# Performance work log

Hardware: AMD Instinct MI355X
Metric: run time of the kernel (lower is better)

The kernel has to match this reference:

```python
import jax, jax.numpy as jnp
import numpy as np

B, T, D, H = 4, 1024, 512, 8
DK = D // H
L = 2 * T - 1  # relative-position length, Transformer-XL convention


def setup_inputs() -> dict:
    key = jax.random.key(0)
    ks = jax.random.split(key, 16)
    s = 0.02  # xavier-ish init scale
    inp = {
        "query": jax.random.normal(ks[0], (B, T, D), jnp.float32),
        "key": jax.random.normal(ks[1], (B, T, D), jnp.float32),
        "value": jax.random.normal(ks[2], (B, T, D), jnp.float32),
        "pos_embedding": jax.random.normal(ks[3], (B, L, D), jnp.float32),
        "mask": jax.random.randint(ks[4], (B, T), 0, 2).astype(bool),
        # nn.Linear weights are [out, in]; y = x @ W.T + b
        "Wq": jax.random.normal(ks[5], (D, D), jnp.float32) * s,
        "bq": jnp.zeros((D,), jnp.float32),
        "Wk": jax.random.normal(ks[6], (D, D), jnp.float32) * s,
        "bk": jnp.zeros((D,), jnp.float32),
        "Wv": jax.random.normal(ks[7], (D, D), jnp.float32) * s,
        "bv": jnp.zeros((D,), jnp.float32),
        "Wr": jax.random.normal(ks[8], (D, D), jnp.float32) * s,  # rpe_proj, no bias
        "u_bias": jax.random.normal(ks[9], (H, DK), jnp.float32) * s,
        "v_bias": jax.random.normal(ks[10], (H, DK), jnp.float32) * s,
        "Wo": jax.random.normal(ks[11], (D, D), jnp.float32) * s,
        "bo": jnp.zeros((D,), jnp.float32),
    }
    return inp


def _rel_shift(x):
    # x: [B, H, T, L] -> Transformer-XL pad/reshape/slice shift, keep first L//2+1 cols
    b, h, t, l = x.shape
    x = jnp.pad(x, ((0, 0), (0, 0), (0, 0), (1, 0)))        # [B,H,T,L+1]
    x = x.reshape(b, h, l + 1, t)[:, :, 1:, :]               # drop first row
    x = x.reshape(b, h, t, l)
    return x[..., : l // 2 + 1]                              # [B,H,T,T]


def reference(query, key, value, pos_embedding, mask,
              Wq, bq, Wk, bk, Wv, bv, Wr, u_bias, v_bias, Wo, bo):
    b = query.shape[0]
    q = (query @ Wq.T + bq).reshape(b, -1, H, DK)            # [B,T,H,dk]
    k = (key @ Wk.T + bk).reshape(b, -1, H, DK)              # [B,T,H,dk]
    v = (value @ Wv.T + bv).reshape(b, -1, H, DK)            # [B,T,H,dk]
    r = (pos_embedding @ Wr.T).reshape(b, -1, H, DK)         # [B,L,H,dk]

    main = jnp.einsum('bthd,bshd->bhts', q + u_bias, k)      # content score
    rpe = jnp.einsum('bthd,blhd->bhtl', q + v_bias, r)       # [B,H,T,L]

    scores = (main + _rel_shift(rpe)) / np.sqrt(DK).astype(np.float32)
    scores = jnp.where(mask[:, None, None, :],
                       jnp.asarray(1e-4, scores.dtype), scores)
    attn = jax.nn.softmax(scores, axis=-1)                   # dropout off (eval)

    out = jnp.einsum('bhts,bshd->bhtd', attn, v)             # [B,H,T,dk]
    # Faithful to original: view(B,-1,d_model) WITHOUT transposing heads back
    out = out.reshape(b, -1, D)                              # [B,T,D] (head-interleaved)
    return out @ Wo.T + bo
```

## Files before the change

kernel.cpp:

```cpp
#include <hip/hip_runtime.h>
#include <stdint.h>
#include <stddef.h>

#define B_ 4
#define T_ 1024
#define D_ 512
#define H_ 8
#define DK_ 64
#define L_ 2047
#define LP_ 2048

typedef __attribute__((ext_vector_type(8))) short short8;
typedef __attribute__((ext_vector_type(4))) short short4_t;
typedef __attribute__((ext_vector_type(4))) float f32x4;
typedef __attribute__((ext_vector_type(4))) unsigned int u32x4;
typedef __attribute__((ext_vector_type(8))) __bf16 bf16x8;

static __device__ __forceinline__ short f2bf(float f) {
  union { float f; unsigned u; } x; x.f = f;
  unsigned r = x.u + 0x7fffu + ((x.u >> 16) & 1u);
  return (short)(r >> 16);
}

static __device__ __forceinline__ unsigned cvtpk(float lo, float hi) {
  unsigned r;
  asm("v_cvt_pk_bf16_f32 %0, %1, %2" : "=v"(r) : "v"(lo), "v"(hi));
  return r;
}

static __device__ __forceinline__ f32x4 mfma16(bf16x8 a, bf16x8 b, f32x4 c) {
  return __builtin_amdgcn_mfma_f32_16x16x32_bf16(a, b, c, 0, 0, 0);
}

static __device__ __forceinline__ bf16x8 ldbf8(const short* p) {
  return *(const bf16x8*)p;
}

__global__ __launch_bounds__(256) void convertW_kernel(
    const float* __restrict__ Wq, const float* __restrict__ Wk, const float* __restrict__ Wv,
    const float* __restrict__ Wr, const float* __restrict__ Wo,
    const unsigned char* __restrict__ mraw,
    short* __restrict__ W_bf, float* __restrict__ mask_f)
{
  if (blockIdx.x == 1280) {
    __shared__ int fmis, fany;
    if (threadIdx.x == 0) { fmis = 0; fany = 0; }
    __syncthreads();
    int lm = 0, la = 0;
    for (int i = threadIdx.x; i < B_ * T_; i += 256) {
      unsigned char c = mraw[i];
      if (c) { la = 1; if (i & 3) lm = 1; }
    }
    if (lm) atomicOr(&fmis, 1);
    if (la) atomicOr(&fany, 1);
    __syncthreads();
    int mmode = fmis ? 0 : (fany ? 1 : 2);
    const int* mi = (const int*)mraw;
    for (int i = threadIdx.x; i < B_ * T_; i += 256) {
      int mv = (mmode == 0) ? (int)mraw[i] : (mmode == 1 ? mi[i] : 0);
      mask_f[i] = mv ? 1.0f : 0.0f;
    }
    return;
  }
  int gid = blockIdx.x * 256 + threadIdx.x;
  const float* src; int base;
  if      (gid <  65536) { src = Wq; base = 0; }
  else if (gid < 131072) { src = Wk; base = 65536; }
  else if (gid < 196608) { src = Wv; base = 131072; }
  else if (gid < 262144) { src = Wr; base = 196608; }
  else                   { src = Wo; base = 262144; }
  f32x4 val = ((const f32x4*)src)[gid - base];
  short4_t o;
  o[0] = f2bf(val[0]); o[1] = f2bf(val[1]); o[2] = f2bf(val[2]); o[3] = f2bf(val[3]);
  ((short4_t*)W_bf)[gid] = o;
}

template<int VARIANT>
__global__ __launch_bounds__(256) void proj_gemm(
    const float* __restrict__ qin, const float* __restrict__ kin,
    const float* __restrict__ vin, const float* __restrict__ pin,
    const short* __restrict__ W_bf, const short* __restrict__ ao_bf,
    short* __restrict__ quO, short* __restrict__ qvO, short* __restrict__ khO,
    short* __restrict__ vtO, short* __restrict__ rhO, float* __restrict__ outF,
    const float* __restrict__ bq, const float* __restrict__ bk_,
    const float* __restrict__ bv_, const float* __restrict__ bo_,
    const float* __restrict__ ub, const float* __restrict__ vb)
{
  const int bid0 = blockIdx.x;
  constexpr int PER = (VARIANT == 0) ? 160 : 32;
  const int bid = (bid0 & 7) * PER + (bid0 >> 3);

  const float* Afp = nullptr; const short* Abf = nullptr; const short* W;
  int Mtotal, mode, m0, n0;
  if constexpr (VARIANT == 0) {
    if (bid < 768) {
      int zz = bid >> 8, r2 = bid & 255;
      m0 = (r2 >> 3) * 128; n0 = (r2 & 7) * 64;
      Afp = (zz == 0) ? qin : (zz == 1) ? kin : vin;
      W = W_bf + (size_t)zz * 262144;
      Mtotal = 4096; mode = zz;
    } else {
      int r2 = bid - 768;
      m0 = (r2 >> 3) * 128; n0 = (r2 & 7) * 64;
      Afp = pin; W = W_bf + 786432;
      Mtotal = 8188; mode = 3;
    }
  } else {
    m0 = (bid >> 3) * 128; n0 = (bid & 7) * 64;
    Abf = ao_bf; W = W_bf + 1048576;
    Mtotal = 4096; mode = 4;
  }
  __shared__ __align__(16) short As[2][128 * 64];
  __shared__ __align__(16) short Bs[2][64 * 64];
  const int tid = threadIdx.x;
  const int lane = tid & 63, wid = tid >> 6;
  const int wr = wid >> 1, wc = wid & 1;
  const int l15 = lane & 15, l4 = lane >> 4;
  const int trow = tid >> 3;
  const int s8 = tid & 7;
  const int tcolsw = ((s8 ^ (trow & 7)) << 3);
  const int wbase = wid * 512;

  f32x4 va[4][2];
  auto LOADA = [&](int kt) {
#pragma unroll
    for (int j = 0; j < 4; j++) {
      int srow = m0 + j * 32 + trow; if (srow > Mtotal - 1) srow = Mtotal - 1;
      const f32x4* p = (const f32x4*)(Afp + (size_t)srow * 512 + kt + s8 * 8);
      va[j][0] = p[0]; va[j][1] = p[1];
    }
  };
  auto WRITEA = [&](int buf) {
#pragma unroll
    for (int j = 0; j < 4; j++) {
      u32x4 wv;
      wv[0] = cvtpk(va[j][0][0], va[j][0][1]);
      wv[1] = cvtpk(va[j][0][2], va[j][0][3]);
      wv[2] = cvtpk(va[j][1][0], va[j][1][1]);
      wv[3] = cvtpk(va[j][1][2], va[j][1][3]);
      *(u32x4*)&As[buf][(j * 32 + trow) * 64 + tcolsw] = wv;
    }
  };
  auto STAGEA1 = [&](int buf, int kt) {
#pragma unroll
    for (int j = 0; j < 4; j++) {
      int srow = m0 + j * 32 + trow; if (srow > 4095) srow = 4095;
      __builtin_amdgcn_global_load_lds(
          (const __attribute__((address_space(1))) unsigned int*)(Abf + (size_t)srow * 512 + kt + tcolsw),
          (__attribute__((address_space(3))) unsigned int*)(&As[buf][j * 2048 + wbase]), 16, 0, 0);
    }
  };
  auto STAGEW = [&](int buf, int kt) {
#pragma unroll
    for (int j = 0; j < 2; j++) {
      int row = j * 32 + trow;
      __builtin_amdgcn_global_load_lds(
          (const __attribute__((address_space(1))) unsigned int*)(W + (size_t)(n0 + row) * 512 + kt + tcolsw),
          (__attribute__((address_space(3))) unsigned int*)(&Bs[buf][j * 2048 + wbase]), 16, 0, 0);
    }
  };

  f32x4 acc[4][2] = {};
  if constexpr (VARIANT == 0) { LOADA(0); STAGEW(0, 0); WRITEA(0); }
  else                        { STAGEA1(0, 0); STAGEW(0, 0); }
  __syncthreads();

  for (int it = 0; it < 8; ++it) {
    const int cur = it & 1;
    if (it < 7) {
      if constexpr (VARIANT == 0) { LOADA((it + 1) * 64); STAGEW(cur ^ 1, (it + 1) * 64); }
      else                        { STAGEA1(cur ^ 1, (it + 1) * 64); STAGEW(cur ^ 1, (it + 1) * 64); }
    }
    __builtin_amdgcn_s_setprio(1);
#pragma unroll
    for (int kf = 0; kf < 2; kf++) {
      const int colA = ((kf * 4 + l4) ^ (l15 & 7)) << 3;
      bf16x8 af[4], bf2[2];
#pragma unroll
      for (int rf = 0; rf < 4; rf++)
        af[rf] = ldbf8(&As[cur][(wr * 64 + rf * 16 + l15) * 64 + colA]);
#pragma unroll
      for (int cf = 0; cf < 2; cf++)
        bf2[cf] = ldbf8(&Bs[cur][(wc * 32 + cf * 16 + l15) * 64 + colA]);
#pragma unroll
      for (int rf = 0; rf < 4; rf++)
#pragma unroll
        for (int cf = 0; cf < 2; cf++)
          acc[rf][cf] = mfma16(af[rf], bf2[cf], acc[rf][cf]);
    }
    __builtin_amdgcn_s_setprio(0);
    if constexpr (VARIANT == 0) { if (it < 7) WRITEA(cur ^ 1); }
    __syncthreads();
  }

#pragma unroll
  for (int cf = 0; cf < 2; cf++) {
    int n = n0 + wc * 32 + cf * 16 + l15;
    float bias = 0.f, ubv = 0.f, vbv = 0.f;
    if (mode == 0) { bias = bq[n]; ubv = ub[n]; vbv = vb[n]; }
    else if (mode == 1) bias = bk_[n];
    else if (mode == 2) bias = bv_[n];
    else if (mode == 4) bias = bo_[n];
    int hh = n >> 6, dk = n & 63;
#pragma unroll
    for (int rf = 0; rf < 4; rf++) {
#pragma unroll
      for (int reg = 0; reg < 4; reg++) {
        int m = m0 + wr * 64 + rf * 16 + l4 * 4 + reg;
        float val = acc[rf][cf][reg] + bias;
        if (mode == 0) {
          int bb = m >> 10, t = m & 1023;
          size_t ad = ((size_t)(bb * H_ + hh) * T_ + t) * DK_ + dk;
          quO[ad] = f2bf(val + ubv);
          qvO[ad] = f2bf(val + vbv);
        } else if (mode == 1) {
          int bb = m >> 10, t = m & 1023;
          khO[((size_t)(bb * H_ + hh) * T_ + t) * DK_ + dk] = f2bf(val);
        } else if (mode == 2) {
          int bb = m >> 10, t = m & 1023;
          vtO[((size_t)(bb * H_ + hh) * DK_ + dk) * T_ + t] = f2bf(val);
        } else if (mode == 3) {
          if (m < B_ * L_) {
            int bb = m / L_;
            int ll = m - bb * L_;
            rhO[((size_t)(bb * H_ + hh) * LP_ + ll) * DK_ + dk] = f2bf(val);
          }
        } else {
          outF[(size_t)m * D_ + n] = val;
        }
      }
    }
  }
}

__global__ __launch_bounds__(256) void attn_kernel(
    const short* __restrict__ qu, const short* __restrict__ qv,
    const short* __restrict__ kh, const short* __restrict__ vt,
    const short* __restrict__ rh, const float* __restrict__ mask_f,
    short* __restrict__ attnout)
{
  const int tid = threadIdx.x;
  const int lane = tid & 63;
  const int w = tid >> 6;
  const int l15 = lane & 15, l4 = lane >> 4;
  const int bid = blockIdx.x;
  const int xcd = bid & 7, slot = bid >> 3;
  const int bh = (slot >> 4) * 8 + xcd;
  const int b = bh >> 3;
  const int t0b = (slot & 15) * 64;
  const int t0w = t0b + w * 16;
  const int woff = 48 - w * 16;

  __shared__ __align__(16) short Ks[2][64 * 64];
  __shared__ __align__(16) short Vs[2][64 * 64];
  __shared__ __align__(16) short Rs[2][128 * 64];
  __shared__ __align__(16) short Ps[4][16 * 64];

  const short* kB = kh + (size_t)bh * T_ * DK_;
  const short* vB = vt + (size_t)bh * DK_ * T_;
  const short* rB = rh + (size_t)bh * LP_ * DK_;
  const float* mB = mask_f + b * T_;

  const short* quB = qu + ((size_t)bh * T_ + t0w + l15) * DK_ + l4 * 8;
  const short* qvB = qv + ((size_t)bh * T_ + t0w + l15) * DK_ + l4 * 8;
  bf16x8 quf0 = ldbf8(quB), quf1 = ldbf8(quB + 32);
  bf16x8 qvf0 = ldbf8(qvB), qvf1 = ldbf8(qvB + 32);

  const short8 ones_s = {(short)0x3F80, (short)0x3F80, (short)0x3F80, (short)0x3F80,
                         (short)0x3F80, (short)0x3F80, (short)0x3F80, (short)0x3F80};
  const bf16x8 ones8 = __builtin_bit_cast(bf16x8, ones_s);

  const int trow = tid >> 3;
  const int tcol = (((tid & 7) ^ ((tid >> 3) & 7)) << 3);
  const int wbase = w * 512;

  auto STAGE = [&](int buf, int s0) {
    const int l0b = 960 + s0 - t0b;
#pragma unroll
    for (int j = 0; j < 2; j++) {
      __builtin_amdgcn_global_load_lds(
          (const __attribute__((address_space(1))) unsigned int*)(kB + (size_t)(s0 + trow + j * 32) * 64 + tcol),
          (__attribute__((address_space(3))) unsigned int*)(&Ks[buf][j * 2048 + wbase]), 16, 0, 0);
      __builtin_amdgcn_global_load_lds(
          (const __attribute__((address_space(1))) unsigned int*)(vB + (size_t)(trow + j * 32) * T_ + s0 + tcol),
          (__attribute__((address_space(3))) unsigned int*)(&Vs[buf][j * 2048 + wbase]), 16, 0, 0);
    }
#pragma unroll
    for (int j = 0; j < 4; j++) {
      __builtin_amdgcn_global_load_lds(
          (const __attribute__((address_space(1))) unsigned int*)(rB + (size_t)(l0b + trow + j * 32) * 64 + tcol),
          (__attribute__((address_space(3))) unsigned int*)(&Rs[buf][j * 2048 + wbase]), 16, 0, 0);
    }
  };

  f32x4 accO[4] = {};
  f32x4 sum_acc = {};

  STAGE(0, 0);
  __syncthreads();

  const int swz = (l15 & 7) << 3;

  for (int it = 0; it < 16; ++it) {
    const int s0 = it << 6;
    const int cur = it & 1;
    if (it < 15) STAGE(cur ^ 1, s0 + 64);

    float mk[4];
#pragma unroll
    for (int cf = 0; cf < 4; cf++) mk[cf] = mB[s0 + cf * 16 + l15];

    f32x4 sacc[4] = {};
    f32x4 gacc[5] = {};
    __builtin_amdgcn_s_setprio(1);
#pragma unroll
    for (int kf = 0; kf < 2; kf++) {
      const int col = (kf * 32 + l4 * 8) ^ swz;
      bf16x8 qf = kf ? quf1 : quf0;
      bf16x8 vf_ = kf ? qvf1 : qvf0;
#pragma unroll
      for (int cf = 0; cf < 4; cf++)
        sacc[cf] = mfma16(qf, ldbf8(&Ks[cur][(cf * 16 + l15) * 64 + col]), sacc[cf]);
#pragma unroll
      for (int gf = 0; gf < 5; gf++)
        gacc[gf] = mfma16(vf_, ldbf8(&Rs[cur][(woff + gf * 16 + l15) * 64 + col]), gacc[gf]);
    }
    __builtin_amdgcn_s_setprio(0);

    float p[4][4];
#pragma unroll
    for (int r = 0; r < 4; r++) {
      const int tl = l4 * 4 + r;
      const int e = l15 + 15 - tl;
      const int src = (lane & 48) | (e & 15);
      float sh0 = __shfl(gacc[0][r], src);
      float sh1 = __shfl(gacc[1][r], src);
      float sh2 = __shfl(gacc[2][r], src);
      float sh3 = __shfl(gacc[3][r], src);
      float sh4 = __shfl(gacc[4][r], src);
      float ga[4] = {sh0, sh1, sh2, sh3};
      float gb[4] = {sh1, sh2, sh3, sh4};
#pragma unroll
      for (int cf = 0; cf < 4; cf++) {
        float gg = (e < 16) ? ga[cf] : gb[cf];
        float lg = (sacc[cf][r] + gg) * 0.125f;
        lg = (mk[cf] != 0.f) ? 1e-4f : lg;
        p[r][cf] = __expf(lg);
      }
    }

#pragma unroll
    for (int r = 0; r < 4; r++) {
      const int tl = l4 * 4 + r;
      const int sw2 = (tl & 7) << 3;
#pragma unroll
      for (int cf = 0; cf < 4; cf++)
        Ps[w][tl * 64 + ((cf * 16 + l15) ^ sw2)] = f2bf(p[r][cf]);
    }

    __builtin_amdgcn_s_setprio(1);
#pragma unroll
    for (int kf = 0; kf < 2; kf++) {
      const int kc = kf * 32 + l4 * 8;
      bf16x8 pa = ldbf8(&Ps[w][l15 * 64 + (kc ^ swz)]);
      sum_acc = mfma16(pa, ones8, sum_acc);
#pragma unroll
      for (int vf = 0; vf < 4; vf++)
        accO[vf] = mfma16(pa, ldbf8(&Vs[cur][(vf * 16 + l15) * 64 + (kc ^ swz)]), accO[vf]);
    }
    __builtin_amdgcn_s_setprio(0);
    __syncthreads();
  }

#pragma unroll
  for (int r = 0; r < 4; r++) {
    const int tl = l4 * 4 + r;
    float inv = 1.0f / sum_acc[r];
#pragma unroll
    for (int vf = 0; vf < 4; vf++) {
      float val = accO[vf][r] * inv;
      attnout[((size_t)bh * T_ + t0w + tl) * DK_ + vf * 16 + l15] = f2bf(val);
    }
  }
}

extern "C" void kernel_launch(void* const* d_in, const int* in_sizes, int n_in,
                              void* d_out, int out_size, void* d_ws, size_t ws_size,
                              hipStream_t stream) {
  const float* qin = (const float*)d_in[0];
  const float* kin = (const float*)d_in[1];
  const float* vin = (const float*)d_in[2];
  const float* pin = (const float*)d_in[3];
  const unsigned char* mraw = (const unsigned char*)d_in[4];
  const float* Wq = (const float*)d_in[5];
  const float* bq = (const float*)d_in[6];
  const float* Wk = (const float*)d_in[7];
  const float* bk = (const float*)d_in[8];
  const float* Wv = (const float*)d_in[9];
  const float* bv = (const float*)d_in[10];
  const float* Wr = (const float*)d_in[11];
  const float* ub = (const float*)d_in[12];
  const float* vb = (const float*)d_in[13];
  const float* Wo = (const float*)d_in[14];
  const float* bo = (const float*)d_in[15];
  float* out = (float*)d_out;
  char* ws = (char*)d_ws;

  short* W_bf   = (short*)(ws + 20967424);
  float* mask_f = (float*)(ws + 23588864);
  short* quW    = (short*)(ws + 23605248);
  short* qvW    = (short*)(ws + 27799552);
  short* khW    = (short*)(ws + 31993856);
  short* vtW    = (short*)(ws + 36188160);
  short* rhW    = (short*)(ws + 40382464);
  short* aoW    = (short*)(ws + 48771072);

  convertW_kernel<<<dim3(1281), dim3(256), 0, stream>>>(
      Wq, Wk, Wv, Wr, Wo, mraw, W_bf, mask_f);
  proj_gemm<0><<<dim3(1280), dim3(256), 0, stream>>>(
      qin, kin, vin, pin, W_bf, aoW, quW, qvW, khW, vtW, rhW, nullptr,
      bq, bk, bv, bo, ub, vb);
  attn_kernel<<<dim3(512), dim3(256), 0, stream>>>(
      quW, qvW, khW, vtW, rhW, mask_f, aoW);
  proj_gemm<1><<<dim3(256), dim3(256), 0, stream>>>(
      qin, kin, vin, pin, W_bf, aoW, quW, qvW, khW, vtW, rhW, out,
      bq, bk, bv, bo, ub, vb);
}
```

Measured before the change: 97.12 us.

## Load projection weights directly into registers instead of staging through LDS

The projection GEMM no longer stages the weight tile in shared memory. Each lane now loads its MFMA B-fragments straight from global memory into registers, which drops the Bs buffer and halves LDS use. The Wo variant switches from async global_load_lds to register loads followed by LDS writes, the k-loop is fully unrolled, and launch bounds now request 4 blocks per CU for higher occupancy. In exchange, the weight loads are issued in the same iteration that consumes them, so their latency is no longer hidden by the double buffer, and register pressure rises.

```diff
diff --git a/kernel.cpp b/kernel.cpp
--- a/kernel.cpp
+++ b/kernel.cpp
@@ -76,7 +76,7 @@
 }
 
 template<int VARIANT>
-__global__ __launch_bounds__(256) void proj_gemm(
+__global__ __launch_bounds__(256, 4) void proj_gemm(
     const float* __restrict__ qin, const float* __restrict__ kin,
     const float* __restrict__ vin, const float* __restrict__ pin,
     const short* __restrict__ W_bf, const short* __restrict__ ao_bf,
@@ -111,7 +111,6 @@
     Mtotal = 4096; mode = 4;
   }
   __shared__ __align__(16) short As[2][128 * 64];
-  __shared__ __align__(16) short Bs[2][64 * 64];
   const int tid = threadIdx.x;
   const int lane = tid & 63, wid = tid >> 6;
   const int wr = wid >> 1, wc = wid & 1;
@@ -119,77 +118,78 @@
   const int trow = tid >> 3;
   const int s8 = tid & 7;
   const int tcolsw = ((s8 ^ (trow & 7)) << 3);
-  const int wbase = wid * 512;
+
+  const short* Wp0 = W + (size_t)(n0 + wc * 32 + l15) * 512 + l4 * 8;
+  const short* Wp1 = W + (size_t)(n0 + wc * 32 + 16 + l15) * 512 + l4 * 8;
 
   f32x4 va[4][2];
+  bf16x8 va1[4];
+  bf16x8 wf[2][2];
+
   auto LOADA = [&](int kt) {
-#pragma unroll
-    for (int j = 0; j < 4; j++) {
-      int srow = m0 + j * 32 + trow; if (srow > Mtotal - 1) srow = Mtotal - 1;
-      const f32x4* p = (const f32x4*)(Afp + (size_t)srow * 512 + kt + s8 * 8);
-      va[j][0] = p[0]; va[j][1] = p[1];
-    }
+    if constexpr (VARIANT == 0) {
+#pragma unroll
+      for (int j = 0; j < 4; j++) {
+        int srow = m0 + j * 32 + trow; if (srow > Mtotal - 1) srow = Mtotal - 1;
+        const f32x4* p = (const f32x4*)(Afp + (size_t)srow * 512 + kt + s8 * 8);
+        va[j][0] = p[0]; va[j][1] = p[1];
+      }
+    } else {
+#pragma unroll
+      for (int j = 0; j < 4; j++) {
+        int srow = m0 + j * 32 + trow; if (srow > 4095) srow = 4095;
+        va1[j] = ldbf8(Abf + (size_t)srow * 512 + kt + s8 * 8);
+      }
+    }
+  };
+  auto LOADW = [&](int kt) {
+    wf[0][0] = ldbf8(Wp0 + kt);      wf[0][1] = ldbf8(Wp1 + kt);
+    wf[1][0] = ldbf8(Wp0 + kt + 32); wf[1][1] = ldbf8(Wp1 + kt + 32);
   };
   auto WRITEA = [&](int buf) {
-#pragma unroll
-    for (int j = 0; j < 4; j++) {
-      u32x4 wv;
-      wv[0] = cvtpk(va[j][0][0], va[j][0][1]);
-      wv[1] = cvtpk(va[j][0][2], va[j][0][3]);
-      wv[2] = cvtpk(va[j][1][0], va[j][1][1]);
-      wv[3] = cvtpk(va[j][1][2], va[j][1][3]);
-      *(u32x4*)&As[buf][(j * 32 + trow) * 64 + tcolsw] = wv;
+    if constexpr (VARIANT == 0) {
+#pragma unroll
+      for (int j = 0; j < 4; j++) {
+        u32x4 wv;
+        wv[0] = cvtpk(va[j][0][0], va[j][0][1]);
+        wv[1] = cvtpk(va[j][0][2], va[j][0][3]);
+        wv[2] = cvtpk(va[j][1][0], va[j][1][1]);
+        wv[3] = cvtpk(va[j][1][2], va[j][1][3]);
+        *(u32x4*)&As[buf][(j * 32 + trow) * 64 + tcolsw] = wv;
+      }
+    } else {
+#pragma unroll
+      for (int j = 0; j < 4; j++)
+        *(bf16x8*)&As[buf][(j * 32 + trow) * 64 + tcolsw] = va1[j];
     }
   };
-  auto STAGEA1 = [&](int buf, int kt) {
-#pragma unroll
-    for (int j = 0; j < 4; j++) {
-      int srow = m0 + j * 32 + trow; if (srow > 4095) srow = 4095;
-      __builtin_amdgcn_global_load_lds(
-          (const __attribute__((address_space(1))) unsigned int*)(Abf + (size_t)srow * 512 + kt + tcolsw),
-          (__attribute__((address_space(3))) unsigned int*)(&As[buf][j * 2048 + wbase]), 16, 0, 0);
-    }
-  };
-  auto STAGEW = [&](int buf, int kt) {
-#pragma unroll
-    for (int j = 0; j < 2; j++) {
-      int row = j * 32 + trow;
-      __builtin_amdgcn_global_load_lds(
-          (const __attribute__((address_space(1))) unsigned int*)(W + (size_t)(n0 + row) * 512 + kt + tcolsw),
-          (__attribute__((address_space(3))) unsigned int*)(&Bs[buf][j * 2048 + wbase]), 16, 0, 0);
-    }
-  };
 
   f32x4 acc[4][2] = {};
-  if constexpr (VARIANT == 0) { LOADA(0); STAGEW(0, 0); WRITEA(0); }
-  else                        { STAGEA1(0, 0); STAGEW(0, 0); }
+  LOADA(0);
+  WRITEA(0);
   __syncthreads();
 
+#pragma unroll
   for (int it = 0; it < 8; ++it) {
     const int cur = it & 1;
-    if (it < 7) {
-      if constexpr (VARIANT == 0) { LOADA((it + 1) * 64); STAGEW(cur ^ 1, (it + 1) * 64); }
-      else                        { STAGEA1(cur ^ 1, (it + 1) * 64); STAGEW(cur ^ 1, (it + 1) * 64); }
-    }
+    LOADW(it * 64);
+    if (it < 7) LOADA((it + 1) * 64);
     __builtin_amdgcn_s_setprio(1);
 #pragma unroll
     for (int kf = 0; kf < 2; kf++) {
       const int colA = ((kf * 4 + l4) ^ (l15 & 7)) << 3;
-      bf16x8 af[4], bf2[2];
+      bf16x8 af[4];
 #pragma unroll
       for (int rf = 0; rf < 4; rf++)
         af[rf] = ldbf8(&As[cur][(wr * 64 + rf * 16 + l15) * 64 + colA]);
 #pragma unroll
-      for (int cf = 0; cf < 2; cf++)
-        bf2[cf] = ldbf8(&Bs[cur][(wc * 32 + cf * 16 + l15) * 64 + colA]);
-#pragma unroll
       for (int rf = 0; rf < 4; rf++)
 #pragma unroll
         for (int cf = 0; cf < 2; cf++)
-          acc[rf][cf] = mfma16(af[rf], bf2[cf], acc[rf][cf]);
+          acc[rf][cf] = mfma16(af[rf], wf[kf][cf], acc[rf][cf]);
     }
     __builtin_amdgcn_s_setprio(0);
-    if constexpr (VARIANT == 0) { if (it < 7) WRITEA(cur ^ 1); }
+    if (it < 7) WRITEA(cur ^ 1);
     __syncthreads();
   }
 
```

After: 107.9 us. 11.1% more time.
